# Optimization experiments

Hardware: AMD Instinct MI355X
Metric: run time of the kernel (lower is better)

Reference implementation:

```python
import jax, jax.numpy as jnp
import numpy as np

B = 16384
# (num_embeddings, embedding_dim, avg_hist) per table
SPECS = [(1_000_000, 64, 50), (100_000, 128, 20), (500_000, 32, 100), (1_000_000, 64, 50)]


def setup_inputs() -> dict:
    key = jax.random.key(0)
    rng = np.random.default_rng(0)
    inp = {}
    for i, (num, dim, hist) in enumerate(SPECS):
        T = B * hist
        kw, ki = jax.random.split(jax.random.fold_in(key, i))
        inp[f"W{i}"] = jax.random.normal(kw, (num, dim), dtype=jnp.float32) * 0.01
        inp[f"ids{i}"] = jax.random.randint(ki, (T,), 0, num, dtype=jnp.int64 if jax.config.jax_enable_x64 else jnp.int32)
        # jagged lengths that sum exactly to T (multinomial over B bins)
        lens = rng.multinomial(T, np.full(B, 1.0 / B))
        inp[f"lens{i}"] = jnp.asarray(lens, dtype=jnp.int32)
    return inp


def _pool(W, ids, lens):
    # sum-pooling embedding_bag: gather rows then segment-sum per bag.
    T = ids.shape[0]
    seg = jnp.repeat(jnp.arange(lens.shape[0]), lens, total_repeat_length=T)  # [T]
    return jax.ops.segment_sum(W[ids], seg, num_segments=lens.shape[0])  # [B, dim]


def reference(W0, W1, W2, W3, ids0, ids1, ids2, ids3, lens0, lens1, lens2, lens3):
    pooled = [
        _pool(W0, ids0, lens0),
        _pool(W1, ids1, lens1),
        _pool(W2, ids2, lens2),
        _pool(W3, ids3, lens3),
    ]
    return jnp.concatenate(pooled, axis=1)  # [B, sum(dims)] = KeyedTensor values
```

## Files before the change

kernel.cpp:

```cpp
#include <hip/hip_runtime.h>
#include <hip/hip_bf16.h>

#define NBAGS 16384
#define OUT_STRIDE 288

struct Ptrs {
    const float* W[4];
    const int* ids[4];
    const int* lens[4];
    int* starts[4];
    float* out;
};

__global__ void __launch_bounds__(256) scan_kernel(Ptrs p) {
    const int t = blockIdx.x >> 8;
    const int c = blockIdx.x & 255;
    const int* __restrict__ lens = p.lens[t];
    int* __restrict__ starts = p.starts[t];
    const int tid = threadIdx.x;
    const int P = c * 64;

    __shared__ int red[256];
    int s = 0;
    for (int k = tid; k < P; k += 256) s += lens[k];
    red[tid] = s;
    __syncthreads();
    for (int off = 128; off > 0; off >>= 1) {
        if (tid < off) red[tid] += red[tid + off];
        __syncthreads();
    }
    const int prefix = red[0];

    if (tid < 64) {
        const int v = lens[P + tid];
        int inc = v;
#pragma unroll
        for (int off = 1; off < 64; off <<= 1) {
            int u = __shfl_up(inc, off, 64);
            if (tid >= off) inc += u;
        }
        starts[P + tid] = prefix + inc - v;
    }
}

template <int D, int UNROLL>
__device__ __forceinline__ void pool_bags(
    const float* __restrict__ W, const int* __restrict__ ids,
    const int* __restrict__ starts, const int* __restrict__ lens,
    float* __restrict__ out, int col_off, int blk)
{
    constexpr int TPB = D / 4;
    constexpr int BAGS = 256 / TPB;
    constexpr int RS = D / 4;

    const int bag = blk * BAGS + threadIdx.x / TPB;
    const int lane = threadIdx.x % TPB;
    const int s = starts[bag];
    const int n = lens[bag];
    const float4* __restrict__ Wl = reinterpret_cast<const float4*>(W) + lane;

    float4 acc[UNROLL];
#pragma unroll
    for (int u = 0; u < UNROLL; ++u) acc[u] = make_float4(0.f, 0.f, 0.f, 0.f);

    int j = 0;
    for (; j + UNROLL <= n; j += UNROLL) {
        int idx[UNROLL];
#pragma unroll
        for (int u = 0; u < UNROLL; ++u) idx[u] = ids[s + j + u];
#pragma unroll
        for (int u = 0; u < UNROLL; ++u) {
            const float4 v = Wl[(size_t)idx[u] * RS];
            acc[u].x += v.x; acc[u].y += v.y; acc[u].z += v.z; acc[u].w += v.w;
        }
    }
    for (; j < n; ++j) {
        const float4 v = Wl[(size_t)ids[s + j] * RS];
        acc[0].x += v.x; acc[0].y += v.y; acc[0].z += v.z; acc[0].w += v.w;
    }

#pragma unroll
    for (int u = 1; u < UNROLL; ++u) {
        acc[0].x += acc[u].x; acc[0].y += acc[u].y;
        acc[0].z += acc[u].z; acc[0].w += acc[u].w;
    }

    float4* __restrict__ o = reinterpret_cast<float4*>(
        out + (size_t)bag * OUT_STRIDE + col_off) + lane;
    *o = acc[0];
}

#define B0 1024
#define B1 3072
#define B2 3584
#define B3 4608

__global__ void __launch_bounds__(256) pool_fused(Ptrs p) {
    const int b = blockIdx.x;
    if (b < B0) {
        pool_bags<64, 8>(p.W[0], p.ids[0], p.starts[0], p.lens[0], p.out, 0, b);
    } else if (b < B1) {
        pool_bags<128, 8>(p.W[1], p.ids[1], p.starts[1], p.lens[1], p.out, 64, b - B0);
    } else if (b < B2) {
        pool_bags<32, 8>(p.W[2], p.ids[2], p.starts[2], p.lens[2], p.out, 192, b - B1);
    } else {
        pool_bags<64, 8>(p.W[3], p.ids[3], p.starts[3], p.lens[3], p.out, 224, b - B2);
    }
}

extern "C" void kernel_launch(void* const* d_in, const int* in_sizes, int n_in,
                              void* d_out, int out_size, void* d_ws, size_t ws_size,
                              hipStream_t stream) {
    Ptrs p;
    for (int t = 0; t < 4; ++t) {
        p.W[t]    = (const float*)d_in[3 * t + 0];
        p.ids[t]  = (const int*)d_in[3 * t + 1];
        p.lens[t] = (const int*)d_in[3 * t + 2];
        p.starts[t] = (int*)d_ws + t * NBAGS;
    }
    p.out = (float*)d_out;

    scan_kernel<<<1024, 256, 0, stream>>>(p);
    pool_fused<<<B3, 256, 0, stream>>>(p);
}
```

Measured before the change: 146.3 us.

## Split long bags across thread groups and interleave tables across blocks

Each bag is now processed by G thread groups that stride over its indices, with G chosen per table (more for tables with longer histories). Partial sums are reduced through shared memory before writing. Blocks are interleaved across the four tables so every block handles eight bags of one table, balancing per-block work. The tail loop is replaced by a predicated unrolled pass that issues clamped redundant loads. This adds a block barrier and shared-memory traffic.

```diff
diff --git a/kernel.cpp b/kernel.cpp
--- a/kernel.cpp
+++ b/kernel.cpp
@@ -43,18 +43,19 @@
     }
 }
 
-template <int D, int UNROLL>
-__device__ __forceinline__ void pool_bags(
+template <int D, int G, int UNROLL>
+__device__ __forceinline__ void pool_unit(
     const float* __restrict__ W, const int* __restrict__ ids,
     const int* __restrict__ starts, const int* __restrict__ lens,
-    float* __restrict__ out, int col_off, int blk)
+    float* __restrict__ out, int col_off, int chunk, float4* sm)
 {
     constexpr int TPB = D / 4;
-    constexpr int BAGS = 256 / TPB;
-    constexpr int RS = D / 4;
-
-    const int bag = blk * BAGS + threadIdx.x / TPB;
-    const int lane = threadIdx.x % TPB;
+    constexpr int SLOTS = 256 / (TPB * G);
+    const int tid = threadIdx.x;
+    const int slot = tid / (TPB * G);
+    const int g = (tid / TPB) % G;
+    const int lane = tid % TPB;
+    const int bag = chunk * SLOTS + slot;
     const int s = starts[bag];
     const int n = lens[bag];
     const float4* __restrict__ Wl = reinterpret_cast<const float4*>(W) + lane;
@@ -63,20 +64,33 @@
 #pragma unroll
     for (int u = 0; u < UNROLL; ++u) acc[u] = make_float4(0.f, 0.f, 0.f, 0.f);
 
-    int j = 0;
-    for (; j + UNROLL <= n; j += UNROLL) {
+    int j = g;
+    for (; j + (UNROLL - 1) * G < n; j += UNROLL * G) {
         int idx[UNROLL];
 #pragma unroll
-        for (int u = 0; u < UNROLL; ++u) idx[u] = ids[s + j + u];
+        for (int u = 0; u < UNROLL; ++u) idx[u] = ids[s + j + u * G];
 #pragma unroll
         for (int u = 0; u < UNROLL; ++u) {
-            const float4 v = Wl[(size_t)idx[u] * RS];
+            const float4 v = Wl[(size_t)idx[u] * TPB];
             acc[u].x += v.x; acc[u].y += v.y; acc[u].z += v.z; acc[u].w += v.w;
         }
     }
-    for (; j < n; ++j) {
-        const float4 v = Wl[(size_t)ids[s + j] * RS];
-        acc[0].x += v.x; acc[0].y += v.y; acc[0].z += v.z; acc[0].w += v.w;
+    if (j < n) {
+        int idx[UNROLL];
+        bool ok[UNROLL];
+#pragma unroll
+        for (int u = 0; u < UNROLL; ++u) {
+            const int jj = j + u * G;
+            ok[u] = (jj < n);
+            idx[u] = ids[s + (ok[u] ? jj : (n - 1))];
+        }
+#pragma unroll
+        for (int u = 0; u < UNROLL; ++u) {
+            const float4 v = Wl[(size_t)idx[u] * TPB];
+            if (ok[u]) {
+                acc[u].x += v.x; acc[u].y += v.y; acc[u].z += v.z; acc[u].w += v.w;
+            }
+        }
     }
 
 #pragma unroll
@@ -85,26 +99,33 @@
         acc[0].z += acc[u].z; acc[0].w += acc[u].w;
     }
 
-    float4* __restrict__ o = reinterpret_cast<float4*>(
-        out + (size_t)bag * OUT_STRIDE + col_off) + lane;
-    *o = acc[0];
+    if constexpr (G == 1) {
+        float4* o = reinterpret_cast<float4*>(out + (size_t)bag * OUT_STRIDE + col_off) + lane;
+        *o = acc[0];
+    } else {
+        sm[tid] = acc[0];
+        __syncthreads();
+        if (g == 0) {
+#pragma unroll
+            for (int h = 1; h < G; ++h) {
+                const float4 v = sm[tid + h * TPB];
+                acc[0].x += v.x; acc[0].y += v.y; acc[0].z += v.z; acc[0].w += v.w;
+            }
+            float4* o = reinterpret_cast<float4*>(out + (size_t)bag * OUT_STRIDE + col_off) + lane;
+            *o = acc[0];
+        }
+    }
 }
 
-#define B0 1024
-#define B1 3072
-#define B2 3584
-#define B3 4608
-
 __global__ void __launch_bounds__(256) pool_fused(Ptrs p) {
-    const int b = blockIdx.x;
-    if (b < B0) {
-        pool_bags<64, 8>(p.W[0], p.ids[0], p.starts[0], p.lens[0], p.out, 0, b);
-    } else if (b < B1) {
-        pool_bags<128, 8>(p.W[1], p.ids[1], p.starts[1], p.lens[1], p.out, 64, b - B0);
-    } else if (b < B2) {
-        pool_bags<32, 8>(p.W[2], p.ids[2], p.starts[2], p.lens[2], p.out, 192, b - B1);
-    } else {
-        pool_bags<64, 8>(p.W[3], p.ids[3], p.starts[3], p.lens[3], p.out, 224, b - B2);
+    __shared__ float4 sm[256];
+    const int u = blockIdx.x;
+    const int chunk = u >> 2;
+    switch (u & 3) {
+    case 0: pool_unit<64, 2, 8>(p.W[0], p.ids[0], p.starts[0], p.lens[0], p.out, 0,   chunk, sm); break;
+    case 1: pool_unit<128, 1, 8>(p.W[1], p.ids[1], p.starts[1], p.lens[1], p.out, 64,  chunk, sm); break;
+    case 2: pool_unit<32, 4, 8>(p.W[2], p.ids[2], p.starts[2], p.lens[2], p.out, 192, chunk, sm); break;
+    default: pool_unit<64, 2, 8>(p.W[3], p.ids[3], p.starts[3], p.lens[3], p.out, 224, chunk, sm); break;
     }
 }
 
@@ -121,5 +142,5 @@
     p.out = (float*)d_out;
 
     scan_kernel<<<1024, 256, 0, stream>>>(p);
-    pool_fused<<<B3, 256, 0, stream>>>(p);
+    pool_fused<<<NBAGS / 8 * 4, 256, 0, stream>>>(p);
 }
```

Result: faster. 137.8 us (-5.8%).

## Map one wavefront per bag with scalar-address batched gathers and interleaved table blocks

Applied to the files above, without the earlier changes.

Restructures pooling so each 64-lane wavefront handles a whole bag, with bag start and length made wave-uniform via readfirstlane. Row base addresses go in scalar registers for inline-asm global loads, issued in batches of 16 (or 8) followed by a single waitcnt. Tail elements are masked with fmaf. The 32-wide table packs two bags per wave, and blocks from the four tables are interleaved in the grid to balance load. This aims to raise memory-level parallelism and cut per-thread address arithmetic, at the cost of wasted loads on tail iterations and inline-asm fragility.

```diff
diff --git a/kernel.cpp b/kernel.cpp
--- a/kernel.cpp
+++ b/kernel.cpp
@@ -3,6 +3,8 @@
 
 #define NBAGS 16384
 #define OUT_STRIDE 288
+
+typedef float v2f __attribute__((ext_vector_type(2)));
 
 struct Ptrs {
     const float* W[4];
@@ -43,68 +45,156 @@
     }
 }
 
-template <int D, int UNROLL>
-__device__ __forceinline__ void pool_bags(
-    const float* __restrict__ W, const int* __restrict__ ids,
-    const int* __restrict__ starts, const int* __restrict__ lens,
-    float* __restrict__ out, int col_off, int blk)
+__device__ __forceinline__ int rfl(int x) { return __builtin_amdgcn_readfirstlane(x); }
+
+__device__ __forceinline__ void wave_d64(const float* __restrict__ W,
+    const int* __restrict__ ids, int s, int n, float* __restrict__ op, int lane)
 {
-    constexpr int TPB = D / 4;
-    constexpr int BAGS = 256 / TPB;
-    constexpr int RS = D / 4;
-
-    const int bag = blk * BAGS + threadIdx.x / TPB;
-    const int lane = threadIdx.x % TPB;
-    const int s = starts[bag];
-    const int n = lens[bag];
-    const float4* __restrict__ Wl = reinterpret_cast<const float4*>(W) + lane;
-
-    float4 acc[UNROLL];
-#pragma unroll
-    for (int u = 0; u < UNROLL; ++u) acc[u] = make_float4(0.f, 0.f, 0.f, 0.f);
-
+    const unsigned loff = (unsigned)lane * 4u;
+    float a0 = 0.f, a1 = 0.f, a2 = 0.f, a3 = 0.f;
     int j = 0;
-    for (; j + UNROLL <= n; j += UNROLL) {
-        int idx[UNROLL];
-#pragma unroll
-        for (int u = 0; u < UNROLL; ++u) idx[u] = ids[s + j + u];
-#pragma unroll
-        for (int u = 0; u < UNROLL; ++u) {
-            const float4 v = Wl[(size_t)idx[u] * RS];
-            acc[u].x += v.x; acc[u].y += v.y; acc[u].z += v.z; acc[u].w += v.w;
+    while (j < n) {
+        float r0, r1, r2, r3, r4, r5, r6, r7, r8, r9, r10, r11, r12, r13, r14, r15;
+#define ISS64(k)                                                              \
+        { const int jj = j + k; const int ix = (jj < n) ? jj : (n - 1);       \
+          const float* p_ = W + (size_t)ids[s + ix] * 64;                     \
+          asm volatile("global_load_dword %0, %1, %2"                         \
+                       : "=v"(r##k) : "v"(loff), "s"(p_)); }
+        ISS64(0) ISS64(1) ISS64(2) ISS64(3) ISS64(4) ISS64(5) ISS64(6) ISS64(7)
+        ISS64(8) ISS64(9) ISS64(10) ISS64(11) ISS64(12) ISS64(13) ISS64(14) ISS64(15)
+#undef ISS64
+        asm volatile("s_waitcnt vmcnt(0)");
+        __builtin_amdgcn_sched_barrier(0);
+        if (j + 16 <= n) {
+            a0 += r0;  a1 += r1;  a2 += r2;  a3 += r3;
+            a0 += r4;  a1 += r5;  a2 += r6;  a3 += r7;
+            a0 += r8;  a1 += r9;  a2 += r10; a3 += r11;
+            a0 += r12; a1 += r13; a2 += r14; a3 += r15;
+        } else {
+#define ACM64(k, d)                                                           \
+            { const float m_ = (j + k < n) ? 1.f : 0.f;                       \
+              a##d = fmaf(m_, r##k, a##d); }
+            ACM64(0,0) ACM64(1,1) ACM64(2,2) ACM64(3,3)
+            ACM64(4,0) ACM64(5,1) ACM64(6,2) ACM64(7,3)
+            ACM64(8,0) ACM64(9,1) ACM64(10,2) ACM64(11,3)
+            ACM64(12,0) ACM64(13,1) ACM64(14,2) ACM64(15,3)
+#undef ACM64
         }
-    }
-    for (; j < n; ++j) {
-        const float4 v = Wl[(size_t)ids[s + j] * RS];
-        acc[0].x += v.x; acc[0].y += v.y; acc[0].z += v.z; acc[0].w += v.w;
-    }
-
-#pragma unroll
-    for (int u = 1; u < UNROLL; ++u) {
-        acc[0].x += acc[u].x; acc[0].y += acc[u].y;
-        acc[0].z += acc[u].z; acc[0].w += acc[u].w;
-    }
-
-    float4* __restrict__ o = reinterpret_cast<float4*>(
-        out + (size_t)bag * OUT_STRIDE + col_off) + lane;
-    *o = acc[0];
-}
-
-#define B0 1024
-#define B1 3072
-#define B2 3584
-#define B3 4608
+        j += 16;
+    }
+    op[lane] = (a0 + a1) + (a2 + a3);
+}
+
+__device__ __forceinline__ void wave_d128(const float* __restrict__ W,
+    const int* __restrict__ ids, int s, int n, float* __restrict__ op, int lane)
+{
+    const unsigned loff = (unsigned)lane * 8u;
+    v2f a0 = {0.f, 0.f}, a1 = {0.f, 0.f}, a2 = {0.f, 0.f}, a3 = {0.f, 0.f};
+    int j = 0;
+    while (j < n) {
+        v2f r0, r1, r2, r3, r4, r5, r6, r7;
+#define ISS128(k)                                                             \
+        { const int jj = j + k; const int ix = (jj < n) ? jj : (n - 1);       \
+          const float* p_ = W + (size_t)ids[s + ix] * 128;                    \
+          asm volatile("global_load_dwordx2 %0, %1, %2"                       \
+                       : "=v"(r##k) : "v"(loff), "s"(p_)); }
+        ISS128(0) ISS128(1) ISS128(2) ISS128(3)
+        ISS128(4) ISS128(5) ISS128(6) ISS128(7)
+#undef ISS128
+        asm volatile("s_waitcnt vmcnt(0)");
+        __builtin_amdgcn_sched_barrier(0);
+        if (j + 8 <= n) {
+            a0 += r0; a1 += r1; a2 += r2; a3 += r3;
+            a0 += r4; a1 += r5; a2 += r6; a3 += r7;
+        } else {
+#define ACM128(k, d)                                                          \
+            { const float m_ = (j + k < n) ? 1.f : 0.f;                       \
+              a##d.x = fmaf(m_, r##k.x, a##d.x);                              \
+              a##d.y = fmaf(m_, r##k.y, a##d.y); }
+            ACM128(0,0) ACM128(1,1) ACM128(2,2) ACM128(3,3)
+            ACM128(4,0) ACM128(5,1) ACM128(6,2) ACM128(7,3)
+#undef ACM128
+        }
+        j += 8;
+    }
+    const v2f a = (a0 + a1) + (a2 + a3);
+    *reinterpret_cast<v2f*>(op + lane * 2) = a;
+}
+
+__device__ __forceinline__ void wave_d32x2(const float* __restrict__ W,
+    const int* __restrict__ ids, int sA, int nA, int sB, int nB,
+    float* __restrict__ opA, float* __restrict__ opB, int lane)
+{
+    const int half = lane >> 5;
+    const int l5 = lane & 31;
+    float a0 = 0.f, a1 = 0.f, a2 = 0.f, a3 = 0.f;
+    const int nmax = (nA > nB) ? nA : nB;
+    int j = 0;
+    while (j < nmax) {
+        float r0, r1, r2, r3, r4, r5, r6, r7;
+#define ISS32(k)                                                              \
+        { const int jj = j + k;                                               \
+          const int iA = ids[(nA > 0) ? (sA + ((jj < nA) ? jj : (nA - 1))) : 0]; \
+          const int iB = ids[(nB > 0) ? (sB + ((jj < nB) ? jj : (nB - 1))) : 0]; \
+          const float* pp = W + (size_t)(half ? iB : iA) * 32 + l5;           \
+          asm volatile("global_load_dword %0, %1, off"                        \
+                       : "=v"(r##k) : "v"(pp)); }
+        ISS32(0) ISS32(1) ISS32(2) ISS32(3) ISS32(4) ISS32(5) ISS32(6) ISS32(7)
+#undef ISS32
+        asm volatile("s_waitcnt vmcnt(0)");
+        __builtin_amdgcn_sched_barrier(0);
+#define ACM32(k, d)                                                           \
+        { const float mA_ = (j + k < nA) ? 1.f : 0.f;                         \
+          const float mB_ = (j + k < nB) ? 1.f : 0.f;                         \
+          const float m_ = half ? mB_ : mA_;                                  \
+          a##d = fmaf(m_, r##k, a##d); }
+        ACM32(0,0) ACM32(1,1) ACM32(2,2) ACM32(3,3)
+        ACM32(4,0) ACM32(5,1) ACM32(6,2) ACM32(7,3)
+#undef ACM32
+        j += 8;
+    }
+    const float a = (a0 + a1) + (a2 + a3);
+    (half ? opB : opA)[l5] = a;
+}
 
 __global__ void __launch_bounds__(256) pool_fused(Ptrs p) {
     const int b = blockIdx.x;
-    if (b < B0) {
-        pool_bags<64, 8>(p.W[0], p.ids[0], p.starts[0], p.lens[0], p.out, 0, b);
-    } else if (b < B1) {
-        pool_bags<128, 8>(p.W[1], p.ids[1], p.starts[1], p.lens[1], p.out, 64, b - B0);
-    } else if (b < B2) {
-        pool_bags<32, 8>(p.W[2], p.ids[2], p.starts[2], p.lens[2], p.out, 192, b - B1);
+    const int c = b / 7, r = b % 7;
+    int t, within;
+    switch (r) {
+    case 0: t = 0; within = c * 2;     break;
+    case 1: t = 1; within = c * 2;     break;
+    case 2: t = 2; within = c;         break;
+    case 3: t = 3; within = c * 2;     break;
+    case 4: t = 0; within = c * 2 + 1; break;
+    case 5: t = 1; within = c * 2 + 1; break;
+    default: t = 3; within = c * 2 + 1; break;
+    }
+    const int wid = rfl((int)threadIdx.x >> 6);
+    const int lane = threadIdx.x & 63;
+
+    if (t == 2) {
+        const int pidx = within * 4 + wid;
+        const int bagA = 2 * pidx, bagB = 2 * pidx + 1;
+        const int sA = rfl(p.starts[2][bagA]);
+        const int nA = rfl(p.lens[2][bagA]);
+        const int sB = rfl(p.starts[2][bagB]);
+        const int nB = rfl(p.lens[2][bagB]);
+        wave_d32x2(p.W[2], p.ids[2], sA, nA, sB, nB,
+                   p.out + (size_t)bagA * OUT_STRIDE + 192,
+                   p.out + (size_t)bagB * OUT_STRIDE + 192, lane);
+    } else if (t == 1) {
+        const int bag = within * 4 + wid;
+        const int s = rfl(p.starts[1][bag]);
+        const int n = rfl(p.lens[1][bag]);
+        wave_d128(p.W[1], p.ids[1], s, n,
+                  p.out + (size_t)bag * OUT_STRIDE + 64, lane);
     } else {
-        pool_bags<64, 8>(p.W[3], p.ids[3], p.starts[3], p.lens[3], p.out, 224, b - B2);
+        const int bag = within * 4 + wid;
+        const int s = rfl(p.starts[t][bag]);
+        const int n = rfl(p.lens[t][bag]);
+        wave_d64(p.W[t], p.ids[t], s, n,
+                 p.out + (size_t)bag * OUT_STRIDE + (t == 0 ? 0 : 224), lane);
     }
 }
 
@@ -121,5 +211,5 @@
     p.out = (float*)d_out;
 
     scan_kernel<<<1024, 256, 0, stream>>>(p);
-    pool_fused<<<B3, 256, 0, stream>>>(p);
-}
+    pool_fused<<<7 * 2048, 256, 0, stream>>>(p);
+}
```

Result: no change. 149.2 us (+2.0%).
